# Kernel optimization log

Hardware: AMD Instinct MI355X
Metric: run time of the kernel (lower is better)

Reference implementation:

```python
import jax, jax.numpy as jnp
import numpy as np

B, S, D = 2, 2048, 4096
H, KV, HD = 32, 8, 128          # n_heads, n_kv_heads, head_dim
N_REP = H // KV                  # GQA repeat factor = 4
ROPE_THETA = 500000.0


def _rope_tables(seqlen, head_dim, theta):
    inv_freq = 1.0 / (theta ** (np.arange(0, head_dim, 2, dtype=np.float32) / head_dim))
    angles = np.outer(np.arange(seqlen, dtype=np.float32), inv_freq)  # [S, HD/2]
    return jnp.asarray(np.cos(angles)), jnp.asarray(np.sin(angles))


def setup_inputs() -> dict:
    key = jax.random.key(0)
    ks = jax.random.split(key, 6)
    x = jax.random.normal(ks[0], (B, S, D), dtype=jnp.float32)
    freqs_cos, freqs_sin = _rope_tables(S, HD, ROPE_THETA)
    # causal additive mask, broadcast over (batch, heads)
    mask = jnp.where(jnp.tril(jnp.ones((S, S), dtype=bool)), 0.0, -jnp.inf).astype(jnp.float32)
    sc = 0.02
    wq = sc * jax.random.normal(ks[1], (D, H * HD), dtype=jnp.float32)   # (in, out)
    wk = sc * jax.random.normal(ks[2], (D, KV * HD), dtype=jnp.float32)
    wv = sc * jax.random.normal(ks[3], (D, KV * HD), dtype=jnp.float32)
    wo = sc * jax.random.normal(ks[4], (H * HD, D), dtype=jnp.float32)
    return {"x": x, "freqs_cos": freqs_cos, "freqs_sin": freqs_sin, "mask": mask,
            "wq": wq, "wk": wk, "wv": wv, "wo": wo}


def _apply_rope(t, cos, sin):
    # t: [B, S, nh, HD]; cos/sin: [S, HD/2]. Complex rotation on adjacent pairs.
    t2 = t.reshape(*t.shape[:-1], HD // 2, 2)
    t0, t1 = t2[..., 0], t2[..., 1]
    c = cos[None, :, None, :]
    s = sin[None, :, None, :]
    r0 = t0 * c - t1 * s
    r1 = t0 * s + t1 * c
    return jnp.stack([r0, r1], axis=-1).reshape(t.shape)


def reference(x, freqs_cos, freqs_sin, mask, wq, wk, wv, wo):
    bsz, seqlen, _ = x.shape
    xq = (x @ wq).reshape(bsz, seqlen, H, HD)
    xk = (x @ wk).reshape(bsz, seqlen, KV, HD)
    xv = (x @ wv).reshape(bsz, seqlen, KV, HD)
    xq = _apply_rope(xq, freqs_cos, freqs_sin)
    xk = _apply_rope(xk, freqs_cos, freqs_sin)
    # repeat_kv (GQA) -> [B, S, H, HD]
    keys = jnp.repeat(xk, N_REP, axis=2)
    values = jnp.repeat(xv, N_REP, axis=2)
    scores = jnp.einsum('bqhd,bkhd->bhqk', xq, keys) / jnp.sqrt(jnp.float32(HD))
    scores = scores + mask[None, None, :, :]
    probs = jax.nn.softmax(scores.astype(jnp.float32), axis=-1).astype(xq.dtype)
    out = jnp.einsum('bhqk,bkhd->bqhd', probs, values).reshape(bsz, seqlen, H * HD)
    return out @ wo
```

## Files before the change

### kernel.cpp

```cpp
#include <hip/hip_runtime.h>
#include <stdint.h>

#define B_ 2
#define S_ 2048
#define D_ 4096
#define H_ 32
#define KV_ 8
#define HD_ 128
#define M_ (B_*S_)
#define NQ_ (H_*HD_)
#define NKV_ (KV_*HD_)

typedef unsigned short u16;
typedef __bf16 bf16x8 __attribute__((ext_vector_type(8)));
typedef float f32x4 __attribute__((ext_vector_type(4)));
typedef u16 u16x8 __attribute__((ext_vector_type(8)));
typedef u16 u16x4 __attribute__((ext_vector_type(4)));

__device__ __forceinline__ u16 f2bf(float f) {
  union { float f; unsigned u; } v; v.f = f;
  unsigned r = v.u + 0x7fffu + ((v.u >> 16) & 1u);
  return (u16)(r >> 16);
}
__device__ __forceinline__ u16 f2bft(float f) {
  union { float f; unsigned u; } v; v.f = f;
  return (u16)(v.u >> 16);
}
__device__ __forceinline__ float bf2f(u16 u) {
  union { unsigned u; float f; } v; v.u = ((unsigned)u) << 16;
  return v.f;
}
__device__ __forceinline__ f32x4 mfma16(bf16x8 a, bf16x8 b, f32x4 c) {
  return __builtin_amdgcn_mfma_f32_16x16x32_bf16(a, b, c, 0, 0, 0);
}

#define GLDS16(gp, lp) __builtin_amdgcn_global_load_lds( \
    (const __attribute__((address_space(1))) unsigned int*)(gp), \
    (__attribute__((address_space(3))) unsigned int*)(lp), 16, 0, 0)

__global__ __launch_bounds__(256) void cvt_bf16(const float* __restrict__ in,
                                                u16* __restrict__ out, int n) {
  int i = (blockIdx.x * 256 + threadIdx.x) * 8;
  if (i >= n) return;
  float4 a = *(const float4*)(in + i);
  float4 b = *(const float4*)(in + i + 4);
  u16x8 o;
  o[0]=f2bf(a.x); o[1]=f2bf(a.y); o[2]=f2bf(a.z); o[3]=f2bf(a.w);
  o[4]=f2bf(b.x); o[5]=f2bf(b.y); o[6]=f2bf(b.z); o[7]=f2bf(b.w);
  *(u16x8*)(out + i) = o;
}

__global__ __launch_bounds__(256) void tcvt(const float* __restrict__ in,
                                            u16* __restrict__ out, int R, int C) {
  __shared__ __attribute__((aligned(16))) u16 tile[32][33];
  int c0 = blockIdx.x * 32, r0 = blockIdx.y * 32;
  int tx = threadIdx.x & 31, ty = threadIdx.x >> 5;
  #pragma unroll
  for (int j = ty; j < 32; j += 8)
    tile[j][tx] = f2bf(in[(size_t)(r0 + j) * C + c0 + tx]);
  __syncthreads();
  #pragma unroll
  for (int j = ty; j < 32; j += 8)
    out[(size_t)(c0 + j) * R + r0 + tx] = tile[tx][j];
}

template<int OUTMODE>
__global__ __launch_bounds__(256) void gemm_bt(const u16* __restrict__ A,
    const u16* __restrict__ BT, void* __restrict__ Cv, void* __restrict__ Cv2,
    int M, int N, int K) {
  __shared__ __attribute__((aligned(16))) u16 As[128 * 32];
  __shared__ __attribute__((aligned(16))) u16 Bs[128 * 32];
  const int tid = threadIdx.x;
  const int bn0 = blockIdx.x * 128, bm0 = blockIdx.y * 128;
  const int w = tid >> 6, l = tid & 63, g = l >> 4, q = l & 15;
  const int wm = (w >> 1) * 64, wn = (w & 1) * 64;
  f32x4 acc[4][4] = {};
  for (int kt = 0; kt < K; kt += 32) {
    __syncthreads();
    #pragma unroll
    for (int p = 0; p < 2; ++p) {
      int c = tid + p * 256;
      int row = c >> 2, slot = c & 3;
      int srck = (slot ^ ((row >> 1) & 3)) << 3;
      GLDS16(A + (size_t)(bm0 + row) * K + kt + srck, As + c * 8);
      GLDS16(BT + (size_t)(bn0 + row) * K + kt + srck, Bs + c * 8);
    }
    __syncthreads();
    bf16x8 af[4], bfr[4];
    #pragma unroll
    for (int m = 0; m < 4; ++m) {
      int row = wm + m * 16 + q;
      af[m] = *(const bf16x8*)(As + row * 32 + ((g ^ ((row >> 1) & 3)) << 3));
    }
    #pragma unroll
    for (int n = 0; n < 4; ++n) {
      int row = wn + n * 16 + q;
      bfr[n] = *(const bf16x8*)(Bs + row * 32 + ((g ^ ((row >> 1) & 3)) << 3));
    }
    #pragma unroll
    for (int m = 0; m < 4; ++m)
      #pragma unroll
      for (int n = 0; n < 4; ++n)
        acc[m][n] = mfma16(af[m], bfr[n], acc[m][n]);
  }
  #pragma unroll
  for (int m = 0; m < 4; ++m)
    #pragma unroll
    for (int n = 0; n < 4; ++n) {
      if (OUTMODE == 3) {
        int row0 = bm0 + wm + m * 16 + g * 4;
        int col  = bn0 + wn + n * 16 + q;
        if (col < 1024) {
          #pragma unroll
          for (int j = 0; j < 4; ++j)
            ((u16*)Cv)[(size_t)(row0 + j) * 1024 + col] = f2bf(acc[m][n][j]);
        } else {
          int c2 = col - 1024;
          u16x4 pk;
          #pragma unroll
          for (int j = 0; j < 4; ++j) pk[j] = f2bf(acc[m][n][j]);
          size_t off = ((size_t)((row0 >> 11) * KV_ + (c2 >> 7)) * 32 + ((row0 >> 6) & 31)) * 8192
                     + (size_t)(c2 & 127) * 64 + (row0 & 63);
          *(u16x4*)((u16*)Cv2 + off) = pk;
        }
      } else {
        #pragma unroll
        for (int j = 0; j < 4; ++j) {
          size_t off = (size_t)(bm0 + wm + m * 16 + g * 4 + j) * N + (bn0 + wn + n * 16 + q);
          if (OUTMODE == 1) ((float*)Cv)[off] = acc[m][n][j];
          else              ((u16*)Cv)[off]  = f2bf(acc[m][n][j]);
        }
      }
    }
}

template<int OUTMODE>
__global__ __launch_bounds__(512, 2) void gemm256(const u16* __restrict__ A,
    const u16* __restrict__ BT, void* __restrict__ Cv, int M, int N, int K) {
  extern __shared__ __attribute__((aligned(16))) u16 DL[];
  const int tid = threadIdx.x;
  const int nbx = N >> 8;
  const int cpx = gridDim.x >> 3;
  const int swzb = (blockIdx.x & 7) * cpx + (blockIdx.x >> 3);
  const int bn0 = (swzb % nbx) << 8, bm0 = (swzb / nbx) << 8;
  const int l = tid & 63, g = l >> 4, q = l & 15;
  const int w = tid >> 6;
  const int wm = (w >> 2) * 128, wn = (w & 3) * 64;
  const int nt = K >> 5;
  f32x4 acc[8][4] = {};

  const int srow = tid >> 2, schunk = tid & 3;
  const int ssw = (schunk ^ ((srow >> 1) & 3)) << 3;
  const u16* gA0 = A  + (size_t)(bm0 + srow) * K + ssw;
  const u16* gA1 = gA0 + (size_t)128 * K;
  const u16* gB0 = BT + (size_t)(bn0 + srow) * K + ssw;
  const u16* gB1 = gB0 + (size_t)128 * K;

  auto STAGE = [&](int t) {
    const int kt = t << 5;
    u16* d = DL + (t % 3) * 16384;
    GLDS16(gA0 + kt, d + tid * 8);
    GLDS16(gA1 + kt, d + 4096 + tid * 8);
    GLDS16(gB0 + kt, d + 8192 + tid * 8);
    GLDS16(gB1 + kt, d + 12288 + tid * 8);
  };

  const u16* ra = DL + (wm + q) * 32 + ((g ^ (((wm + q) >> 1) & 3)) << 3);
  const u16* rb = DL + 8192 + (wn + q) * 32 + ((g ^ (((wn + q) >> 1) & 3)) << 3);

  bf16x8 aC[8], aN[8], bC[4], bN[4];

  STAGE(0); STAGE(1);
  asm volatile("s_waitcnt vmcnt(4)" ::: "memory");
  __builtin_amdgcn_s_barrier();
  #pragma unroll
  for (int m = 0; m < 8; ++m) aC[m] = *(const bf16x8*)(ra + m * 512);
  #pragma unroll
  for (int n = 0; n < 4; ++n) bC[n] = *(const bf16x8*)(rb + n * 512);

  auto TILE = [&](int t, bf16x8 (&ac)[8], bf16x8 (&bc)[4],
                         bf16x8 (&an)[8], bf16x8 (&bn)[4]) {
    if (t + 2 < nt) {
      STAGE(t + 2);
      asm volatile("s_waitcnt vmcnt(4)" ::: "memory");
    } else {
      asm volatile("s_waitcnt vmcnt(0)" ::: "memory");
    }
    __builtin_amdgcn_s_barrier();
    if (t + 1 < nt) {
      const u16* pa = ra + ((t + 1) % 3) * 16384;
      const u16* pb = rb + ((t + 1) % 3) * 16384;
      #pragma unroll
      for (int m = 0; m < 8; ++m) an[m] = *(const bf16x8*)(pa + m * 512);
      #pragma unroll
      for (int n = 0; n < 4; ++n) bn[n] = *(const bf16x8*)(pb + n * 512);
    }
    __builtin_amdgcn_s_setprio(1);
    #pragma unroll
    for (int m = 0; m < 8; ++m) {
      acc[m][0] = mfma16(ac[m], bc[0], acc[m][0]);
      acc[m][1] = mfma16(ac[m], bc[1], acc[m][1]);
      acc[m][2] = mfma16(ac[m], bc[2], acc[m][2]);
      acc[m][3] = mfma16(ac[m], bc[3], acc[m][3]);
    }
    __builtin_amdgcn_s_setprio(0);
  };

  for (int t = 0; t < nt; t += 2) {
    TILE(t,     aC, bC, aN, bN);
    TILE(t + 1, aN, bN, aC, bC);
  }

  #pragma unroll
  for (int m = 0; m < 8; ++m)
    #pragma unroll
    for (int n = 0; n < 4; ++n)
      #pragma unroll
      for (int j = 0; j < 4; ++j) {
        size_t off = (size_t)(bm0 + wm + m * 16 + g * 4 + j) * N + (bn0 + wn + n * 16 + q);
        if (OUTMODE == 1) ((float*)Cv)[off] = acc[m][n][j];
        else              ((u16*)Cv)[off]  = f2bf(acc[m][n][j]);
      }
}

__global__ __launch_bounds__(256) void rope_kernel(u16* __restrict__ t,
    const float* __restrict__ fc, const float* __restrict__ fs,
    int log2ppr, int total_pairs) {
  int i = blockIdx.x * 256 + threadIdx.x;
  if (i >= total_pairs) return;
  int fi = i & 63;
  int row = i >> log2ppr;
  int pos = row & (S_ - 1);
  float c = fc[pos * 64 + fi], s = fs[pos * 64 + fi];
  unsigned* p = (unsigned*)(t + 2 * (size_t)i);
  unsigned v = *p;
  float x0 = bf2f((u16)(v & 0xffffu)), x1 = bf2f((u16)(v >> 16));
  float r0 = x0 * c - x1 * s, r1 = x0 * s + x1 * c;
  *p = (unsigned)f2bf(r0) | ((unsigned)f2bf(r1) << 16);
}

__global__ __launch_bounds__(256, 4) void attn_kernel(
    const u16* __restrict__ Qb, const u16* __restrict__ Kb,
    const u16* __restrict__ VTg, u16* __restrict__ Ob) {
  __shared__ __attribute__((aligned(16))) u16 SM[20480];
  u16* Ks = SM;
  u16* Vs = SM + 8192;
  u16* Ps = SM + 16384;
  const int pr = blockIdx.x;
  const int h = blockIdx.y, b = blockIdx.z;
  const int kvh = h >> 2;
  const int tid = threadIdx.x, w = tid >> 6, l = tid & 63, g = l >> 4, ql = l & 15;
  const float SL2E = 0.08838834764831845f * 1.4426950408889634f;
  const u16* Qh = Qb + (size_t)b * S_ * NQ_ + h * HD_;
  const u16* Kh = Kb + ((size_t)b * S_ * KV_ + kvh) * HD_;
  const u16* Vh = VTg + (size_t)(b * KV_ + kvh) * (32 * 8192);
  u16* Oh = Ob + (size_t)b * S_ * NQ_ + h * HD_;

  for (int ph = 0; ph < 2; ++ph) {
    const int qt = ph ? pr : 31 - pr;
    __syncthreads();
    bf16x8 aq[4];
    #pragma unroll
    for (int kk = 0; kk < 4; ++kk)
      aq[kk] = *(const bf16x8*)(Qh + (size_t)(qt * 64 + w * 16 + ql) * NQ_ + kk * 32 + g * 8);

    f32x4 o[8] = {};
    float mrow = -3.0e38f, lrow = 0.f;

    const int nkt = qt + 1;
    for (int kt = 0; kt < nkt; ++kt) {
      #pragma unroll
      for (int p = 0; p < 4; ++p) {
        int c = tid + p * 256;
        int row = c >> 4, slot = c & 15;
        GLDS16(Kh + (size_t)(kt * 64 + row) * (KV_ * HD_) + ((slot ^ (row & 7)) << 3), Ks + c * 8);
      }
      #pragma unroll
      for (int p = 0; p < 4; ++p) {
        int c = tid + p * 256;
        int row = c >> 3, slot = c & 7;
        GLDS16(Vh + (size_t)kt * 8192 + row * 64 + ((slot ^ (row & 7)) << 3), Vs + c * 8);
      }
      asm volatile("s_waitcnt vmcnt(0)" ::: "memory");
      __builtin_amdgcn_s_barrier();

      if (kt * 64 <= qt * 64 + w * 16 + 15) {
        f32x4 sc[4] = {};
        #pragma unroll
        for (int kk = 0; kk < 4; ++kk) {
          bf16x8 bk[4];
          #pragma unroll
          for (int n = 0; n < 4; ++n) {
            int row = n * 16 + ql;
            bk[n] = *(const bf16x8*)(Ks + row * 128 + (((kk * 4 + g) ^ (row & 7)) << 3));
          }
          #pragma unroll
          for (int n = 0; n < 4; ++n)
            sc[n] = mfma16(bk[n], aq[kk], sc[n]);
        }
        const int qglob = qt * 64 + w * 16 + ql;
        if (kt * 64 + 63 > qt * 64 + w * 16) {
          #pragma unroll
          for (int n = 0; n < 4; ++n)
            #pragma unroll
            for (int j = 0; j < 4; ++j)
              if (kt * 64 + n * 16 + g * 4 + j > qglob) sc[n][j] = -3.0e38f;
        }
        float mx = sc[0][0];
        #pragma unroll
        for (int n = 0; n < 4; ++n)
          #pragma unroll
          for (int j = 0; j < 4; ++j) mx = fmaxf(mx, sc[n][j]);
        mx = fmaxf(mx, __shfl_xor(mx, 16));
        mx = fmaxf(mx, __shfl_xor(mx, 32));
        if (!__all(mx - mrow <= 16.0f)) {
          float mnew = fmaxf(mrow, mx);
          float f = exp2f((mrow - mnew) * SL2E);
          lrow *= f;
          #pragma unroll
          for (int m = 0; m < 8; ++m) o[m] *= f;
          mrow = mnew;
        }
        float rs = 0.f;
        #pragma unroll
        for (int n = 0; n < 4; ++n)
          #pragma unroll
          for (int j = 0; j < 4; ++j) {
            float pv = exp2f((sc[n][j] - mrow) * SL2E);
            sc[n][j] = pv; rs += pv;
          }
        rs += __shfl_xor(rs, 16);
        rs += __shfl_xor(rs, 32);
        lrow += rs;
        u16* Pw = Ps + w * 1024;
        #pragma unroll
        for (int n = 0; n < 4; ++n) {
          u16x4 pk;
          #pragma unroll
          for (int j = 0; j < 4; ++j) pk[j] = f2bft(sc[n][j]);
          *(u16x4*)(Pw + ql * 64 + (((n * 2 + (g >> 1)) ^ (ql & 7)) << 3) + (g & 1) * 4) = pk;
        }
        #pragma unroll
        for (int kk2 = 0; kk2 < 2; ++kk2) {
          bf16x8 bp = *(const bf16x8*)(Pw + ql * 64 + (((kk2 * 4 + g) ^ (ql & 7)) << 3));
          #pragma unroll
          for (int m = 0; m < 8; ++m) {
            int row = m * 16 + ql;
            bf16x8 av = *(const bf16x8*)(Vs + row * 64 + (((kk2 * 4 + g) ^ (row & 7)) << 3));
            o[m] = mfma16(av, bp, o[m]);
          }
        }
      }
      __builtin_amdgcn_s_barrier();
    }
    __syncthreads();
    u16* OS = SM;
    float linv = 1.0f / lrow;
    #pragma unroll
    for (int m = 0; m < 8; ++m)
      #pragma unroll
      for (int j = 0; j < 4; ++j)
        OS[(w * 16 + ql) * 136 + m * 16 + g * 4 + j] = f2bf(o[m][j] * linv);
    __syncthreads();
    #pragma unroll
    for (int p = 0; p < 4; ++p) {
      int c = tid + p * 256;
      int row = c >> 4, col8 = c & 15;
      u16x8 d = *(const u16x8*)(OS + row * 136 + col8 * 8);
      *(u16x8*)(Oh + (size_t)(qt * 64 + row) * NQ_ + col8 * 8) = d;
    }
  }
}

extern "C" void kernel_launch(void* const* d_in, const int* in_sizes, int n_in,
                              void* d_out, int out_size, void* d_ws, size_t ws_size,
                              hipStream_t stream) {
  const float* x  = (const float*)d_in[0];
  const float* fc = (const float*)d_in[1];
  const float* fs = (const float*)d_in[2];
  const float* wq = (const float*)d_in[4];
  const float* wk = (const float*)d_in[5];
  const float* wv = (const float*)d_in[6];
  const float* wo = (const float*)d_in[7];

  char* ws = (char*)d_ws;
  u16* xb  = (u16*)(ws + 0);
  u16* wqT = (u16*)(ws + 33554432);
  u16* wkT = (u16*)(ws + 67108864);
  u16* wvT = (u16*)(ws + 75497472);
  u16* woT = (u16*)(ws + 83886080);
  u16* qb  = (u16*)(ws + 117440512);
  u16* kb  = (u16*)(ws + 150994944);
  u16* vtg = (u16*)(ws + 159383552);
  u16* ob  = (u16*)(ws + 167772160);
  if (ws_size < 201326592u) return;

  cvt_bf16<<<(M_ * D_) / (8 * 256), 256, 0, stream>>>(x, xb, M_ * D_);
  tcvt<<<dim3(NQ_ / 32, D_ / 32), 256, 0, stream>>>(wq, wqT, D_, NQ_);
  tcvt<<<dim3(NKV_ / 32, D_ / 32), 256, 0, stream>>>(wk, wkT, D_, NKV_);
  tcvt<<<dim3(NKV_ / 32, D_ / 32), 256, 0, stream>>>(wv, wvT, D_, NKV_);
  tcvt<<<dim3(D_ / 32, NQ_ / 32), 256, 0, stream>>>(wo, woT, NQ_, D_);

  gemm256<0><<<(NQ_ / 256) * (M_ / 256), 512, 98304, stream>>>(xb, wqT, qb, M_, NQ_, D_);
  gemm_bt<3><<<dim3(2048 / 128, M_ / 128), 256, 0, stream>>>(xb, wkT, kb, vtg, M_, 2048, D_);

  rope_kernel<<<(M_ * NQ_ / 2) / 256, 256, 0, stream>>>(qb, fc, fs, 11, M_ * NQ_ / 2);
  rope_kernel<<<(M_ * NKV_ / 2) / 256, 256, 0, stream>>>(kb, fc, fs, 9, M_ * NKV_ / 2);

  attn_kernel<<<dim3(16, H_, B_), 256, 0, stream>>>(qb, kb, vtg, ob);

  gemm256<1><<<(D_ / 256) * (M_ / 256), 512, 98304, stream>>>(ob, woT, d_out, M_, D_, NQ_);
}
```

Measured before the change: 580.4 us.

## Replace K/V GEMM with pipelined 256x128 kernel and vectorize weight transpose

```diff
diff --git a/kernel.cpp b/kernel.cpp
--- a/kernel.cpp
+++ b/kernel.cpp
@@ -52,86 +52,25 @@
 
 __global__ __launch_bounds__(256) void tcvt(const float* __restrict__ in,
                                             u16* __restrict__ out, int R, int C) {
-  __shared__ __attribute__((aligned(16))) u16 tile[32][33];
-  int c0 = blockIdx.x * 32, r0 = blockIdx.y * 32;
-  int tx = threadIdx.x & 31, ty = threadIdx.x >> 5;
-  #pragma unroll
-  for (int j = ty; j < 32; j += 8)
-    tile[j][tx] = f2bf(in[(size_t)(r0 + j) * C + c0 + tx]);
+  __shared__ float tf[64][65];
+  int c0 = blockIdx.x * 64, r0 = blockIdx.y * 64;
+  int l16 = threadIdx.x & 15, r16 = threadIdx.x >> 4;
+  #pragma unroll
+  for (int p = 0; p < 4; ++p) {
+    int r = p * 16 + r16;
+    float4 v = *(const float4*)(in + (size_t)(r0 + r) * C + c0 + l16 * 4);
+    tf[r][l16 * 4 + 0] = v.x; tf[r][l16 * 4 + 1] = v.y;
+    tf[r][l16 * 4 + 2] = v.z; tf[r][l16 * 4 + 3] = v.w;
+  }
   __syncthreads();
-  #pragma unroll
-  for (int j = ty; j < 32; j += 8)
-    out[(size_t)(c0 + j) * R + r0 + tx] = tile[tx][j];
-}
-
-template<int OUTMODE>
-__global__ __launch_bounds__(256) void gemm_bt(const u16* __restrict__ A,
-    const u16* __restrict__ BT, void* __restrict__ Cv, void* __restrict__ Cv2,
-    int M, int N, int K) {
-  __shared__ __attribute__((aligned(16))) u16 As[128 * 32];
-  __shared__ __attribute__((aligned(16))) u16 Bs[128 * 32];
-  const int tid = threadIdx.x;
-  const int bn0 = blockIdx.x * 128, bm0 = blockIdx.y * 128;
-  const int w = tid >> 6, l = tid & 63, g = l >> 4, q = l & 15;
-  const int wm = (w >> 1) * 64, wn = (w & 1) * 64;
-  f32x4 acc[4][4] = {};
-  for (int kt = 0; kt < K; kt += 32) {
-    __syncthreads();
-    #pragma unroll
-    for (int p = 0; p < 2; ++p) {
-      int c = tid + p * 256;
-      int row = c >> 2, slot = c & 3;
-      int srck = (slot ^ ((row >> 1) & 3)) << 3;
-      GLDS16(A + (size_t)(bm0 + row) * K + kt + srck, As + c * 8);
-      GLDS16(BT + (size_t)(bn0 + row) * K + kt + srck, Bs + c * 8);
-    }
-    __syncthreads();
-    bf16x8 af[4], bfr[4];
-    #pragma unroll
-    for (int m = 0; m < 4; ++m) {
-      int row = wm + m * 16 + q;
-      af[m] = *(const bf16x8*)(As + row * 32 + ((g ^ ((row >> 1) & 3)) << 3));
-    }
-    #pragma unroll
-    for (int n = 0; n < 4; ++n) {
-      int row = wn + n * 16 + q;
-      bfr[n] = *(const bf16x8*)(Bs + row * 32 + ((g ^ ((row >> 1) & 3)) << 3));
-    }
-    #pragma unroll
-    for (int m = 0; m < 4; ++m)
-      #pragma unroll
-      for (int n = 0; n < 4; ++n)
-        acc[m][n] = mfma16(af[m], bfr[n], acc[m][n]);
-  }
-  #pragma unroll
-  for (int m = 0; m < 4; ++m)
-    #pragma unroll
-    for (int n = 0; n < 4; ++n) {
-      if (OUTMODE == 3) {
-        int row0 = bm0 + wm + m * 16 + g * 4;
-        int col  = bn0 + wn + n * 16 + q;
-        if (col < 1024) {
-          #pragma unroll
-          for (int j = 0; j < 4; ++j)
-            ((u16*)Cv)[(size_t)(row0 + j) * 1024 + col] = f2bf(acc[m][n][j]);
-        } else {
-          int c2 = col - 1024;
-          u16x4 pk;
-          #pragma unroll
-          for (int j = 0; j < 4; ++j) pk[j] = f2bf(acc[m][n][j]);
-          size_t off = ((size_t)((row0 >> 11) * KV_ + (c2 >> 7)) * 32 + ((row0 >> 6) & 31)) * 8192
-                     + (size_t)(c2 & 127) * 64 + (row0 & 63);
-          *(u16x4*)((u16*)Cv2 + off) = pk;
-        }
-      } else {
-        #pragma unroll
-        for (int j = 0; j < 4; ++j) {
-          size_t off = (size_t)(bm0 + wm + m * 16 + g * 4 + j) * N + (bn0 + wn + n * 16 + q);
-          if (OUTMODE == 1) ((float*)Cv)[off] = acc[m][n][j];
-          else              ((u16*)Cv)[off]  = f2bf(acc[m][n][j]);
-        }
-      }
-    }
+  int oc = threadIdx.x >> 2, ch = threadIdx.x & 3;
+  u16x8 o1, o2;
+  #pragma unroll
+  for (int i = 0; i < 8; ++i) o1[i] = f2bf(tf[ch * 16 + i][oc]);
+  #pragma unroll
+  for (int i = 0; i < 8; ++i) o2[i] = f2bf(tf[ch * 16 + 8 + i][oc]);
+  *(u16x8*)(out + (size_t)(c0 + oc) * R + r0 + ch * 16) = o1;
+  *(u16x8*)(out + (size_t)(c0 + oc) * R + r0 + ch * 16 + 8) = o2;
 }
 
 template<int OUTMODE>
@@ -221,6 +160,101 @@
         if (OUTMODE == 1) ((float*)Cv)[off] = acc[m][n][j];
         else              ((u16*)Cv)[off]  = f2bf(acc[m][n][j]);
       }
+}
+
+__global__ __launch_bounds__(512, 2) void gemm_kv(const u16* __restrict__ A,
+    const u16* __restrict__ BT, u16* __restrict__ Ck, u16* __restrict__ Cvt,
+    int M, int N, int K) {
+  extern __shared__ __attribute__((aligned(16))) u16 DL[];
+  const int tid = threadIdx.x;
+  const int nbx = N >> 7;
+  const int cpx = gridDim.x >> 3;
+  const int swzb = (blockIdx.x & 7) * cpx + (blockIdx.x >> 3);
+  const int bn0 = (swzb % nbx) << 7, bm0 = (swzb / nbx) << 8;
+  const int l = tid & 63, g = l >> 4, q = l & 15;
+  const int w = tid >> 6;
+  const int wm = (w >> 2) * 128, wn = (w & 3) * 32;
+  const int nt = K >> 5;
+  f32x4 acc[8][2] = {};
+
+  const int srow = tid >> 2, schunk = tid & 3;
+  const int ssw = (schunk ^ ((srow >> 1) & 3)) << 3;
+  const u16* gA0 = A  + (size_t)(bm0 + srow) * K + ssw;
+  const u16* gA1 = gA0 + (size_t)128 * K;
+  const u16* gB0 = BT + (size_t)(bn0 + srow) * K + ssw;
+
+  auto STAGE = [&](int t) {
+    const int kt = t << 5;
+    u16* d = DL + (t % 3) * 12288;
+    GLDS16(gA0 + kt, d + tid * 8);
+    GLDS16(gA1 + kt, d + 4096 + tid * 8);
+    GLDS16(gB0 + kt, d + 8192 + tid * 8);
+  };
+
+  const u16* ra = DL + (wm + q) * 32 + ((g ^ (((wm + q) >> 1) & 3)) << 3);
+  const u16* rb = DL + 8192 + (wn + q) * 32 + ((g ^ (((wn + q) >> 1) & 3)) << 3);
+
+  bf16x8 aC[8], aN[8], bC[2], bN[2];
+
+  STAGE(0); STAGE(1);
+  asm volatile("s_waitcnt vmcnt(3)" ::: "memory");
+  __builtin_amdgcn_s_barrier();
+  #pragma unroll
+  for (int m = 0; m < 8; ++m) aC[m] = *(const bf16x8*)(ra + m * 512);
+  #pragma unroll
+  for (int n = 0; n < 2; ++n) bC[n] = *(const bf16x8*)(rb + n * 512);
+
+  auto TILE = [&](int t, bf16x8 (&ac)[8], bf16x8 (&bc)[2],
+                         bf16x8 (&an)[8], bf16x8 (&bn)[2]) {
+    if (t + 2 < nt) {
+      STAGE(t + 2);
+      asm volatile("s_waitcnt vmcnt(3)" ::: "memory");
+    } else {
+      asm volatile("s_waitcnt vmcnt(0)" ::: "memory");
+    }
+    __builtin_amdgcn_s_barrier();
+    if (t + 1 < nt) {
+      const u16* pa = ra + ((t + 1) % 3) * 12288;
+      const u16* pb = rb + ((t + 1) % 3) * 12288;
+      #pragma unroll
+      for (int m = 0; m < 8; ++m) an[m] = *(const bf16x8*)(pa + m * 512);
+      #pragma unroll
+      for (int n = 0; n < 2; ++n) bn[n] = *(const bf16x8*)(pb + n * 512);
+    }
+    __builtin_amdgcn_s_setprio(1);
+    #pragma unroll
+    for (int m = 0; m < 8; ++m) {
+      acc[m][0] = mfma16(ac[m], bc[0], acc[m][0]);
+      acc[m][1] = mfma16(ac[m], bc[1], acc[m][1]);
+    }
+    __builtin_amdgcn_s_setprio(0);
+  };
+
+  for (int t = 0; t < nt; t += 2) {
+    TILE(t,     aC, bC, aN, bN);
+    TILE(t + 1, aN, bN, aC, bC);
+  }
+
+  #pragma unroll
+  for (int m = 0; m < 8; ++m)
+    #pragma unroll
+    for (int n = 0; n < 2; ++n) {
+      int row0 = bm0 + wm + m * 16 + g * 4;
+      int col  = bn0 + wn + n * 16 + q;
+      if (col < 1024) {
+        #pragma unroll
+        for (int j = 0; j < 4; ++j)
+          Ck[(size_t)(row0 + j) * 1024 + col] = f2bf(acc[m][n][j]);
+      } else {
+        int c2 = col - 1024;
+        u16x4 pk;
+        #pragma unroll
+        for (int j = 0; j < 4; ++j) pk[j] = f2bf(acc[m][n][j]);
+        size_t off = ((size_t)((row0 >> 11) * KV_ + (c2 >> 7)) * 32 + ((row0 >> 6) & 31)) * 8192
+                   + (size_t)(c2 & 127) * 64 + (row0 & 63);
+        *(u16x4*)(Cvt + off) = pk;
+      }
+    }
 }
 
 __global__ __launch_bounds__(256) void rope_kernel(u16* __restrict__ t,
@@ -396,13 +430,13 @@
   if (ws_size < 201326592u) return;
 
   cvt_bf16<<<(M_ * D_) / (8 * 256), 256, 0, stream>>>(x, xb, M_ * D_);
-  tcvt<<<dim3(NQ_ / 32, D_ / 32), 256, 0, stream>>>(wq, wqT, D_, NQ_);
-  tcvt<<<dim3(NKV_ / 32, D_ / 32), 256, 0, stream>>>(wk, wkT, D_, NKV_);
-  tcvt<<<dim3(NKV_ / 32, D_ / 32), 256, 0, stream>>>(wv, wvT, D_, NKV_);
-  tcvt<<<dim3(D_ / 32, NQ_ / 32), 256, 0, stream>>>(wo, woT, NQ_, D_);
+  tcvt<<<dim3(NQ_ / 64, D_ / 64), 256, 0, stream>>>(wq, wqT, D_, NQ_);
+  tcvt<<<dim3(NKV_ / 64, D_ / 64), 256, 0, stream>>>(wk, wkT, D_, NKV_);
+  tcvt<<<dim3(NKV_ / 64, D_ / 64), 256, 0, stream>>>(wv, wvT, D_, NKV_);
+  tcvt<<<dim3(D_ / 64, NQ_ / 64), 256, 0, stream>>>(wo, woT, NQ_, D_);
 
   gemm256<0><<<(NQ_ / 256) * (M_ / 256), 512, 98304, stream>>>(xb, wqT, qb, M_, NQ_, D_);
-  gemm_bt<3><<<dim3(2048 / 128, M_ / 128), 256, 0, stream>>>(xb, wkT, kb, vtg, M_, 2048, D_);
+  gemm_kv<<<(2048 / 128) * (M_ / 256), 512, 73728, stream>>>(xb, wkT, kb, vtg, M_, 2048, D_);
 
   rope_kernel<<<(M_ * NQ_ / 2) / 256, 256, 0, stream>>>(qb, fc, fs, 11, M_ * NQ_ / 2);
   rope_kernel<<<(M_ * NKV_ / 2) / 256, 256, 0, stream>>>(kb, fc, fs, 9, M_ * NKV_ / 2);
```

Result: faster. 526.7 us (median of 2 runs) (-9.2%).
